# Kernel tuning notes

Measured on AMD Instinct MI355X. Metric: run time of the kernel, lower is better.

Reference implementation:

```python
import jax, jax.numpy as jnp
import numpy as np
import math

B, T, N_CTX, H = 4, 512, 2048, 1024
NUM_HEADS, NUM_INSTRUMENTS, MAX_BARS = 16, 16, 8
HEAD_DIM = H // NUM_HEADS


def setup_inputs() -> dict:
    key = jax.random.key(0)
    ks = jax.random.split(key, 16)
    s = 1.0 / math.sqrt(H)
    return {
        "query": jax.random.normal(ks[0], (B, T, H), jnp.float32),
        "context": jax.random.normal(ks[1], (B, N_CTX, H), jnp.float32),
        "instrument_ids": jax.random.randint(ks[2], (B, N_CTX), 0, NUM_INSTRUMENTS),
        "current_instrument_id": 3,
        "bar_offsets": jax.random.randint(ks[3], (B, N_CTX), 0, MAX_BARS),
        "Wq": jax.random.normal(ks[4], (H, H), jnp.float32) * s,
        "bq": jnp.zeros((H,), jnp.float32),
        "Wk": jax.random.normal(ks[5], (H, H), jnp.float32) * s,
        "bk": jnp.zeros((H,), jnp.float32),
        "Wv": jax.random.normal(ks[6], (H, H), jnp.float32) * s,
        "bv": jnp.zeros((H,), jnp.float32),
        "Wo": jax.random.normal(ks[7], (H, H), jnp.float32) * s,
        "bo": jnp.zeros((H,), jnp.float32),
        "inst_emb": jax.random.normal(ks[8], (NUM_INSTRUMENTS, H), jnp.float32),
        "bar_emb": jax.random.normal(ks[9], (MAX_BARS, H), jnp.float32),
    }


def reference(query, context, instrument_ids, current_instrument_id, bar_offsets,
              Wq, bq, Wk, bk, Wv, bv, Wo, bo, inst_emb, bar_emb):
    # current_instrument_id: python int -> broadcast to (B,)
    cur = jnp.full((B,), current_instrument_id, dtype=jnp.int64 if instrument_ids.dtype == jnp.int64 else jnp.int32)
    # add embeddings to query and context
    q = query + inst_emb[cur][:, None, :]                              # (B,T,H)
    ctx = context + inst_emb[instrument_ids] + bar_emb[jnp.clip(bar_offsets, 0, MAX_BARS - 1)]  # (B,N,H)
    # projections (torch Linear: x @ W.T + b)
    Q = (q @ Wq.T + bq).reshape(B, T, NUM_HEADS, HEAD_DIM).transpose(0, 2, 1, 3)      # (B,h,T,d)
    K = (ctx @ Wk.T + bk).reshape(B, N_CTX, NUM_HEADS, HEAD_DIM).transpose(0, 2, 1, 3)  # (B,h,N,d)
    V = (ctx @ Wv.T + bv).reshape(B, N_CTX, NUM_HEADS, HEAD_DIM).transpose(0, 2, 1, 3)  # (B,h,N,d)
    scores = jnp.einsum('bhtd,bhnd->bhtn', Q, K) / math.sqrt(HEAD_DIM)  # (B,h,T,N)
    # attend only to keys whose instrument differs from the current one
    keep = (instrument_ids != cur[:, None])[:, None, None, :]           # (B,1,1,N)
    scores = jnp.where(keep, scores, jnp.float32(-1e9))
    probs = jax.nn.softmax(scores, axis=-1)
    out = jnp.einsum('bhtn,bhnd->bhtd', probs, V).transpose(0, 2, 1, 3).reshape(B, T, H)
    return out @ Wo.T + bo
```

## Files before the change

### kernel.cpp

```cpp
#include <hip/hip_runtime.h>

#define H 1024
#define B_ 4
#define T_ 512
#define NCTX 2048
#define NH 16
#define HD 64

typedef __attribute__((ext_vector_type(8))) short bf16x8;
typedef __attribute__((ext_vector_type(4))) float f32x4;
typedef __attribute__((ext_vector_type(4))) short s16x4;

__device__ __forceinline__ ushort f2b(float f) {
  union { float f; unsigned u; } v; v.f = f;
  unsigned u = v.u;
  unsigned r = (u + 0x7FFFu + ((u >> 16) & 1u)) >> 16;
  return (ushort)r;
}

__device__ __forceinline__ unsigned cvt_pk_bf16(float lo, float hi) {
  unsigned r;
  asm("v_cvt_pk_bf16_f32 %0, %1, %2" : "=v"(r) : "v"(lo), "v"(hi));
  return r;
}

__device__ __forceinline__ void gld16(const void* g, void* l) {
  __builtin_amdgcn_global_load_lds((const __attribute__((address_space(1))) unsigned int*)g,
                                   (__attribute__((address_space(3))) unsigned int*)l, 16, 0, 0);
}


__global__ void prep_all(const float* __restrict__ query, const float* __restrict__ ctx,
                         const int* __restrict__ ids, const int* __restrict__ curp,
                         const int* __restrict__ bars,
                         const float* __restrict__ iemb, const float* __restrict__ bemb,
                         const float* __restrict__ Wq, const float* __restrict__ Wk,
                         const float* __restrict__ Wv, const float* __restrict__ Wo,
                         ushort* __restrict__ qin, ushort* __restrict__ ctxb,
                         ushort* __restrict__ Wqb, ushort* __restrict__ Wkb,
                         ushort* __restrict__ Wvb, ushort* __restrict__ Wob,
                         float* __restrict__ maskf) {
  for (int blk = blockIdx.x; blk < 14368; blk += gridDim.x) {
    if (blk < 8192) {
      int i = blk * 256 + threadIdx.x;
      int row = i >> 8;
      int c4 = i & 255;
      int id = ids[row];
      int bar = bars[row];
      bar = bar < 0 ? 0 : (bar > 7 ? 7 : bar);
      float4 v = ((const float4*)ctx)[i];
      float4 e = ((const float4*)(iemb + (size_t)id * H))[c4];
      float4 g = ((const float4*)(bemb + (size_t)bar * H))[c4];
      s16x4 o;
      o[0] = (short)f2b(v.x + e.x + g.x); o[1] = (short)f2b(v.y + e.y + g.y);
      o[2] = (short)f2b(v.z + e.z + g.z); o[3] = (short)f2b(v.w + e.w + g.w);
      ((s16x4*)ctxb)[i] = o;
    } else if (blk < 10240) {
      int cur = curp[0];
      int i = (blk - 8192) * 256 + threadIdx.x;
      int c4 = i & 255;
      float4 v = ((const float4*)query)[i];
      float4 e = ((const float4*)(iemb + (size_t)cur * H))[c4];
      s16x4 o;
      o[0] = (short)f2b(v.x + e.x); o[1] = (short)f2b(v.y + e.y);
      o[2] = (short)f2b(v.z + e.z); o[3] = (short)f2b(v.w + e.w);
      ((s16x4*)qin)[i] = o;
    } else if (blk < 14336) {
      int b2 = blk - 10240;
      int which = b2 >> 10;
      int i = (b2 & 1023) * 256 + threadIdx.x;
      const float* s = which == 0 ? Wq : which == 1 ? Wk : which == 2 ? Wv : Wo;
      ushort* d = which == 0 ? Wqb : which == 1 ? Wkb : which == 2 ? Wvb : Wob;
      float4 v = ((const float4*)s)[i];
      s16x4 o;
      o[0] = (short)f2b(v.x); o[1] = (short)f2b(v.y);
      o[2] = (short)f2b(v.z); o[3] = (short)f2b(v.w);
      ((s16x4*)d)[i] = o;
    } else {
      int cur = curp[0];
      int i = (blk - 14336) * 256 + threadIdx.x;
      maskf[i] = (ids[i] != cur) ? 0.f : -1e30f;
    }
  }
}


__global__ __launch_bounds__(256) void proj_k(const ushort* __restrict__ Aq,
                                              const ushort* __restrict__ Actx,
                                              const ushort* __restrict__ WQ,
                                              const ushort* __restrict__ WK,
                                              const ushort* __restrict__ WV,
                                              const float* __restrict__ bQ,
                                              const float* __restrict__ bK,
                                              const float* __restrict__ bV,
                                              ushort* __restrict__ Qout,
                                              ushort* __restrict__ Kout,
                                              ushort* __restrict__ VTout) {
  const int id = blockIdx.x;
  const ushort* A;
  const ushort* W;
  const float* bias;
  int row0, col0, mode;
  ushort* Cout;
  if (id < 1024) {
    int xcd = id & 7, rest = id >> 3;
    int bx = rest & 15, by = (rest >> 4) * 8 + xcd;
    A = Actx; row0 = by * 128;
    if (bx < 8) { W = WK; bias = bK; col0 = bx * 128; mode = 0; Cout = Kout; }
    else        { W = WV; bias = bV; col0 = (bx - 8) * 128; mode = 1; Cout = VTout; }
  } else {
    int q = id - 1024;
    A = Aq; row0 = (q >> 3) * 128; col0 = (q & 7) * 128;
    W = WQ; bias = bQ; mode = 2; Cout = Qout;
  }

  __shared__ ushort As[2][128 * 32];
  __shared__ ushort Bs[2][128 * 32];
  const int tid = threadIdx.x;
  const int lane = tid & 63;
  const int wv = tid >> 6;
  const int wr = wv >> 1, wc = wv & 1;
  const int lo = lane & 15, hi = lane >> 4;

  f32x4 acc[4][4];
#pragma unroll
  for (int m = 0; m < 4; m++)
#pragma unroll
    for (int n = 0; n < 4; n++) acc[m][n] = (f32x4){0.f, 0.f, 0.f, 0.f};

#pragma unroll
  for (int c = 0; c < 2; c++) {
    int ia = wv * 128 + c * 64 + lane;
    int r = ia >> 2, s = ia & 3;
    gld16(A + (size_t)(row0 + r) * H + s * 8, (char*)As[0] + (wv * 128 + c * 64) * 16);
    gld16(W + (size_t)(col0 + r) * H + s * 8, (char*)Bs[0] + (wv * 128 + c * 64) * 16);
  }
  __syncthreads();

  int cur = 0;
  for (int kt = 0; kt < 32; kt++) {
    if (kt < 31) {
#pragma unroll
      for (int c = 0; c < 2; c++) {
        int ia = wv * 128 + c * 64 + lane;
        int r = ia >> 2, s = ia & 3;
        gld16(A + (size_t)(row0 + r) * H + (kt + 1) * 32 + s * 8,
              (char*)As[cur ^ 1] + (wv * 128 + c * 64) * 16);
        gld16(W + (size_t)(col0 + r) * H + (kt + 1) * 32 + s * 8,
              (char*)Bs[cur ^ 1] + (wv * 128 + c * 64) * 16);
      }
    }
    bf16x8 af[4], bfr[4];
#pragma unroll
    for (int m = 0; m < 4; m++) af[m] = *(const bf16x8*)(As[cur] + (wr * 64 + m * 16 + lo) * 32 + hi * 8);
#pragma unroll
    for (int n = 0; n < 4; n++) bfr[n] = *(const bf16x8*)(Bs[cur] + (wc * 64 + n * 16 + lo) * 32 + hi * 8);
#pragma unroll
    for (int m = 0; m < 4; m++)
#pragma unroll
      for (int n = 0; n < 4; n++)
        acc[m][n] = __builtin_amdgcn_mfma_f32_16x16x32_bf16(af[m], bfr[n], acc[m][n], 0, 0, 0);
    __syncthreads();
    cur ^= 1;
  }

#pragma unroll
  for (int m = 0; m < 4; m++) {
    int gr0 = row0 + wr * 64 + m * 16 + hi * 4;
#pragma unroll
    for (int n = 0; n < 4; n++) {
      int gc = col0 + wc * 64 + n * 16 + lo;
      float bv = bias[gc];
      if (mode == 0) {
#pragma unroll
        for (int r = 0; r < 4; r++)
          Cout[(size_t)(gr0 + r) * H + gc] = f2b(acc[m][n][r] + bv);
      } else if (mode == 1) {
        int bb = gr0 >> 11, n0 = gr0 & 2047;
        s16x4 o;
#pragma unroll
        for (int r = 0; r < 4; r++) o[r] = (short)f2b(acc[m][n][r] + bv);
        *(s16x4*)(Cout + (size_t)bb * (H * NCTX) + (size_t)gc * NCTX + n0) = o;
      } else {
#pragma unroll
        for (int r = 0; r < 4; r++)
          Cout[(size_t)(gr0 + r) * H + gc] = f2b((acc[m][n][r] + bv) * 0.125f);
      }
    }
  }
}


__global__ __launch_bounds__(256) void gemm_o(const ushort* __restrict__ A,
                                              const ushort* __restrict__ W,
                                              const float* __restrict__ bias,
                                              float* __restrict__ Cout) {
  __shared__ ushort As[2][128 * 32];
  __shared__ ushort Bs[2][128 * 32];
  const int tid = threadIdx.x;
  const int lane = tid & 63;
  const int wv = tid >> 6;
  const int wr = wv >> 1, wc = wv & 1;
  const int lo = lane & 15, hi = lane >> 4;
  const int row0 = blockIdx.y * 128, col0 = blockIdx.x * 128;

  f32x4 acc[4][4];
#pragma unroll
  for (int m = 0; m < 4; m++)
#pragma unroll
    for (int n = 0; n < 4; n++) acc[m][n] = (f32x4){0.f, 0.f, 0.f, 0.f};

#pragma unroll
  for (int c = 0; c < 2; c++) {
    int ia = wv * 128 + c * 64 + lane;
    int r = ia >> 2, s = ia & 3;
    gld16(A + (size_t)(row0 + r) * H + s * 8, (char*)As[0] + (wv * 128 + c * 64) * 16);
    gld16(W + (size_t)(col0 + r) * H + s * 8, (char*)Bs[0] + (wv * 128 + c * 64) * 16);
  }
  __syncthreads();

  int cur = 0;
  for (int kt = 0; kt < 32; kt++) {
    if (kt < 31) {
#pragma unroll
      for (int c = 0; c < 2; c++) {
        int ia = wv * 128 + c * 64 + lane;
        int r = ia >> 2, s = ia & 3;
        gld16(A + (size_t)(row0 + r) * H + (kt + 1) * 32 + s * 8,
              (char*)As[cur ^ 1] + (wv * 128 + c * 64) * 16);
        gld16(W + (size_t)(col0 + r) * H + (kt + 1) * 32 + s * 8,
              (char*)Bs[cur ^ 1] + (wv * 128 + c * 64) * 16);
      }
    }
    bf16x8 af[4], bfr[4];
#pragma unroll
    for (int m = 0; m < 4; m++) af[m] = *(const bf16x8*)(As[cur] + (wr * 64 + m * 16 + lo) * 32 + hi * 8);
#pragma unroll
    for (int n = 0; n < 4; n++) bfr[n] = *(const bf16x8*)(Bs[cur] + (wc * 64 + n * 16 + lo) * 32 + hi * 8);
#pragma unroll
    for (int m = 0; m < 4; m++)
#pragma unroll
      for (int n = 0; n < 4; n++)
        acc[m][n] = __builtin_amdgcn_mfma_f32_16x16x32_bf16(af[m], bfr[n], acc[m][n], 0, 0, 0);
    __syncthreads();
    cur ^= 1;
  }

#pragma unroll
  for (int m = 0; m < 4; m++) {
    int gr0 = row0 + wr * 64 + m * 16 + hi * 4;
#pragma unroll
    for (int n = 0; n < 4; n++) {
      int gc = col0 + wc * 64 + n * 16 + lo;
      float bv = bias[gc];
#pragma unroll
      for (int r = 0; r < 4; r++)
        Cout[(size_t)(gr0 + r) * H + gc] = acc[m][n][r] + bv;
    }
  }
}


#define NSPLIT 2
#define KVLEN (NCTX / NSPLIT)
#define NT_KV (KVLEN / 64)

__global__ __launch_bounds__(256) void attn_k(const ushort* __restrict__ Q,
                                              const ushort* __restrict__ K,
                                              const ushort* __restrict__ VT,
                                              const float* __restrict__ maskf,
                                              float* __restrict__ OPf,
                                              float* __restrict__ mlf) {
  __shared__ ushort Ks[2][64 * 64];
  __shared__ ushort Vs[2][64 * 64];
  __shared__ ushort Ps[4][16 * 64];
  const int blk = (blockIdx.x & 7) * 128 + (blockIdx.x >> 3);
  const int qt = blk & 7;
  const int h = (blk >> 3) & 15;
  const int b = (blk >> 7) & 3;
  const int p = blk >> 9;
  const int tid = threadIdx.x, lane = tid & 63, w = tid >> 6;
  const int lo = lane & 15, hi = lane >> 4;
  const int swz = (lo & 7) << 4;
  const int kvbase = p * KVLEN;

  const ushort* Qp = Q + ((size_t)(b * T_ + qt * 64 + w * 16 + lo)) * H + h * HD;
  bf16x8 qf0 = *(const bf16x8*)(Qp + hi * 8);
  bf16x8 qf1 = *(const bf16x8*)(Qp + 32 + hi * 8);

  f32x4 oacc[4];
#pragma unroll
  for (int d = 0; d < 4; d++) oacc[d] = (f32x4){0.f, 0.f, 0.f, 0.f};
  float mrow = -1e30f, lrow = 0.f;

  const float* maskb = maskf + b * NCTX;
  const ushort* Kbase = K + ((size_t)(b * NCTX)) * H + h * HD;
  const ushort* Vbase = VT + (size_t)b * (H * NCTX) + (size_t)(h * HD) * NCTX;

  bf16x8 kr[2], vr[2];
#pragma unroll
  for (int i = 0; i < 2; i++) {
    int seg = tid + i * 256;
    int r = seg >> 3, s = seg & 7;
    kr[i] = *(const bf16x8*)(Kbase + (size_t)(kvbase + r) * H + s * 8);
    vr[i] = *(const bf16x8*)(Vbase + (size_t)r * NCTX + kvbase + s * 8);
  }
#pragma unroll
  for (int i = 0; i < 2; i++) {
    int seg = tid + i * 256;
    int r = seg >> 3, s = seg & 7;
    int wb = (r * 128 + s * 16) ^ ((r & 7) << 4);
    *(bf16x8*)((char*)Ks[0] + wb) = kr[i];
    *(bf16x8*)((char*)Vs[0] + wb) = vr[i];
  }
  __syncthreads();

  int curbuf = 0;
  for (int t = 0; t < NT_KV; t++) {
    int kvt = kvbase + t * 64;
    if (t < NT_KV - 1) {
#pragma unroll
      for (int i = 0; i < 2; i++) {
        int seg = tid + i * 256;
        int r = seg >> 3, s = seg & 7;
        kr[i] = *(const bf16x8*)(Kbase + (size_t)(kvt + 64 + r) * H + s * 8);
        vr[i] = *(const bf16x8*)(Vbase + (size_t)r * NCTX + kvt + 64 + s * 8);
      }
    }

    f32x4 sc[4];
    __builtin_amdgcn_s_setprio(1);
#pragma unroll
    for (int nt = 0; nt < 4; nt++) {
      bf16x8 kf0 = *(const bf16x8*)((char*)Ks[curbuf] + ((((nt * 16 + lo) * 128) + hi * 16) ^ swz));
      bf16x8 kf1 = *(const bf16x8*)((char*)Ks[curbuf] + ((((nt * 16 + lo) * 128) + 64 + hi * 16) ^ swz));
      f32x4 z = (f32x4){0.f, 0.f, 0.f, 0.f};
      z = __builtin_amdgcn_mfma_f32_16x16x32_bf16(kf0, qf0, z, 0, 0, 0);
      sc[nt] = __builtin_amdgcn_mfma_f32_16x16x32_bf16(kf1, qf1, z, 0, 0, 0);
    }
    __builtin_amdgcn_s_setprio(0);

    float pv[4][4];
#pragma unroll
    for (int nt = 0; nt < 4; nt++) {
      float4 mv = *(const float4*)(maskb + kvt + nt * 16 + hi * 4);
      pv[nt][0] = sc[nt][0] + mv.x;
      pv[nt][1] = sc[nt][1] + mv.y;
      pv[nt][2] = sc[nt][2] + mv.z;
      pv[nt][3] = sc[nt][3] + mv.w;
    }

    float m0 = fmaxf(fmaxf(pv[0][0], pv[0][1]), fmaxf(pv[0][2], pv[0][3]));
    float m1 = fmaxf(fmaxf(pv[1][0], pv[1][1]), fmaxf(pv[1][2], pv[1][3]));
    float m2 = fmaxf(fmaxf(pv[2][0], pv[2][1]), fmaxf(pv[2][2], pv[2][3]));
    float m3 = fmaxf(fmaxf(pv[3][0], pv[3][1]), fmaxf(pv[3][2], pv[3][3]));
    float x = fmaxf(fmaxf(m0, m1), fmaxf(m2, m3));
    x = fmaxf(x, __shfl_xor(x, 16));
    x = fmaxf(x, __shfl_xor(x, 32));
    bool defer = __all((x <= mrow + 8.0f) && (mrow > -1e29f));
    float mn, scal = 1.f;
    if (defer) {
      mn = mrow;
    } else {
      mn = fmaxf(mrow, x);
      scal = __expf(mrow - mn);
      mrow = mn;
    }
    float rsp[4];
#pragma unroll
    for (int nt = 0; nt < 4; nt++) {
      float e0 = __expf(pv[nt][0] - mn);
      float e1 = __expf(pv[nt][1] - mn);
      float e2 = __expf(pv[nt][2] - mn);
      float e3 = __expf(pv[nt][3] - mn);
      pv[nt][0] = e0; pv[nt][1] = e1; pv[nt][2] = e2; pv[nt][3] = e3;
      rsp[nt] = (e0 + e1) + (e2 + e3);
    }
    float rs = (rsp[0] + rsp[1]) + (rsp[2] + rsp[3]);
    rs += __shfl_xor(rs, 16);
    rs += __shfl_xor(rs, 32);
    if (defer) {
      lrow += rs;
    } else {
      lrow = lrow * scal + rs;
      float sq0 = __shfl(scal, hi * 4 + 0);
      float sq1 = __shfl(scal, hi * 4 + 1);
      float sq2 = __shfl(scal, hi * 4 + 2);
      float sq3 = __shfl(scal, hi * 4 + 3);
#pragma unroll
      for (int d = 0; d < 4; d++) {
        oacc[d][0] *= sq0; oacc[d][1] *= sq1; oacc[d][2] *= sq2; oacc[d][3] *= sq3;
      }
    }

#pragma unroll
    for (int nt = 0; nt < 4; nt++) {
      uint2 pw;
      pw.x = cvt_pk_bf16(pv[nt][0], pv[nt][1]);
      pw.y = cvt_pk_bf16(pv[nt][2], pv[nt][3]);
      *(uint2*)((char*)Ps[w] + ((lo * 128 + (nt * 16 + hi * 4) * 2) ^ swz)) = pw;
    }

    __builtin_amdgcn_s_setprio(1);
#pragma unroll
    for (int ks = 0; ks < 2; ks++) {
      bf16x8 pa = *(const bf16x8*)((char*)Ps[w] + ((lo * 128 + (ks * 64 + hi * 16)) ^ swz));
#pragma unroll
      for (int d = 0; d < 4; d++) {
        bf16x8 vf = *(const bf16x8*)((char*)Vs[curbuf] + (((d * 16 + lo) * 128 + ks * 64 + hi * 16) ^ swz));
        oacc[d] = __builtin_amdgcn_mfma_f32_16x16x32_bf16(pa, vf, oacc[d], 0, 0, 0);
      }
    }
    __builtin_amdgcn_s_setprio(0);

    if (t < NT_KV - 1) {
#pragma unroll
      for (int i = 0; i < 2; i++) {
        int seg = tid + i * 256;
        int r = seg >> 3, s = seg & 7;
        int wb = (r * 128 + s * 16) ^ ((r & 7) << 4);
        *(bf16x8*)((char*)Ks[curbuf ^ 1] + wb) = kr[i];
        *(bf16x8*)((char*)Vs[curbuf ^ 1] + wb) = vr[i];
      }
    }
    __syncthreads();
    curbuf ^= 1;
  }

  int row0 = b * 512 + qt * 64 + w * 16 + hi * 4;
#pragma unroll
  for (int d = 0; d < 4; d++) {
#pragma unroll
    for (int r = 0; r < 4; r++)
      OPf[((size_t)p * 2048 + row0 + r) * 1024 + h * 64 + d * 16 + lo] = oacc[d][r];
  }
  if (hi == 0) {
    int qrow = b * 512 + qt * 64 + w * 16 + lo;
    mlf[(((size_t)p * 2048 + qrow) * 16 + h) * 2] = mrow;
    mlf[(((size_t)p * 2048 + qrow) * 16 + h) * 2 + 1] = lrow;
  }
}

__global__ void attn_combine(const float* __restrict__ OPf, const float* __restrict__ mlf,
                             ushort* __restrict__ O) {
  int idx = blockIdx.x * 256 + threadIdx.x;
  int btr = idx >> 8;
  int c4 = idx & 255;
  int h = c4 >> 4;
  float m0 = mlf[((size_t)btr * 16 + h) * 2];
  float l0 = mlf[((size_t)btr * 16 + h) * 2 + 1];
  float m1 = mlf[(((size_t)2048 + btr) * 16 + h) * 2];
  float l1 = mlf[(((size_t)2048 + btr) * 16 + h) * 2 + 1];
  float M = fmaxf(m0, m1);
  float a0 = __expf(m0 - M), a1 = __expf(m1 - M);
  float inv = 1.0f / (a0 * l0 + a1 * l1);
  float4 o0 = ((const float4*)OPf)[idx];
  float4 o1 = ((const float4*)OPf)[(size_t)524288 + idx];
  s16x4 r;
  r[0] = (short)f2b((a0 * o0.x + a1 * o1.x) * inv);
  r[1] = (short)f2b((a0 * o0.y + a1 * o1.y) * inv);
  r[2] = (short)f2b((a0 * o0.z + a1 * o1.z) * inv);
  r[3] = (short)f2b((a0 * o0.w + a1 * o1.w) * inv);
  ((s16x4*)O)[idx] = r;
}


extern "C" void kernel_launch(void* const* d_in, const int* in_sizes, int n_in,
                              void* d_out, int out_size, void* d_ws, size_t ws_size,
                              hipStream_t stream) {
  const float* query = (const float*)d_in[0];
  const float* context = (const float*)d_in[1];
  const int* ids = (const int*)d_in[2];
  const int* curp = (const int*)d_in[3];
  const int* bars = (const int*)d_in[4];
  const float* Wq = (const float*)d_in[5];
  const float* bq = (const float*)d_in[6];
  const float* Wk = (const float*)d_in[7];
  const float* bk = (const float*)d_in[8];
  const float* Wv = (const float*)d_in[9];
  const float* bv = (const float*)d_in[10];
  const float* Wo = (const float*)d_in[11];
  const float* bo = (const float*)d_in[12];
  const float* iemb = (const float*)d_in[13];
  const float* bemb = (const float*)d_in[14];
  float* out = (float*)d_out;

  ushort* ws = (ushort*)d_ws;
  ushort* Wqb = ws;
  ushort* Wkb = Wqb + (1u << 20);
  ushort* Wvb = Wkb + (1u << 20);
  ushort* Wob = Wvb + (1u << 20);
  ushort* qin = Wob + (1u << 20);
  ushort* ctxb = qin + (2u << 20);
  ushort* Qb = ctxb + (8u << 20);
  ushort* Kb = Qb + (2u << 20);
  ushort* VTb = Kb + (8u << 20);
  ushort* AOb = VTb + (8u << 20);

  float* OPf = (float*)ctxb;
  float* mlf = (float*)qin;
  float* maskf = out;

  prep_all<<<2048, 256, 0, stream>>>(query, context, ids, curp, bars, iemb, bemb,
                                     Wq, Wk, Wv, Wo, qin, ctxb, Wqb, Wkb, Wvb, Wob, maskf);

  proj_k<<<1152, 256, 0, stream>>>(qin, ctxb, Wqb, Wkb, Wvb, bq, bk, bv, Qb, Kb, VTb);

  attn_k<<<1024, 256, 0, stream>>>(Qb, Kb, VTb, maskf, OPf, mlf);
  attn_combine<<<2048, 256, 0, stream>>>(OPf, mlf, AOb);

  gemm_o<<<dim3(8, 16), 256, 0, stream>>>(AOb, Wob, bo, out);
}
```

Before: 159.0 us.

## Load GEMM operands directly from global memory, dropping LDS staging

```diff
diff --git a/kernel.cpp b/kernel.cpp
--- a/kernel.cpp
+++ b/kernel.cpp
@@ -22,11 +22,6 @@
   unsigned r;
   asm("v_cvt_pk_bf16_f32 %0, %1, %2" : "=v"(r) : "v"(lo), "v"(hi));
   return r;
-}
-
-__device__ __forceinline__ void gld16(const void* g, void* l) {
-  __builtin_amdgcn_global_load_lds((const __attribute__((address_space(1))) unsigned int*)g,
-                                   (__attribute__((address_space(3))) unsigned int*)l, 16, 0, 0);
 }
 
 
@@ -114,8 +109,6 @@
     W = WQ; bias = bQ; mode = 2; Cout = Qout;
   }
 
-  __shared__ ushort As[2][128 * 32];
-  __shared__ ushort Bs[2][128 * 32];
   const int tid = threadIdx.x;
   const int lane = tid & 63;
   const int wv = tid >> 6;
@@ -128,40 +121,28 @@
 #pragma unroll
     for (int n = 0; n < 4; n++) acc[m][n] = (f32x4){0.f, 0.f, 0.f, 0.f};
 
-#pragma unroll
-  for (int c = 0; c < 2; c++) {
-    int ia = wv * 128 + c * 64 + lane;
-    int r = ia >> 2, s = ia & 3;
-    gld16(A + (size_t)(row0 + r) * H + s * 8, (char*)As[0] + (wv * 128 + c * 64) * 16);
-    gld16(W + (size_t)(col0 + r) * H + s * 8, (char*)Bs[0] + (wv * 128 + c * 64) * 16);
-  }
-  __syncthreads();
-
-  int cur = 0;
+  const ushort* Ap[4];
+  const ushort* Wp[4];
+#pragma unroll
+  for (int m = 0; m < 4; m++)
+    Ap[m] = A + (size_t)(row0 + wr * 64 + m * 16 + lo) * H + hi * 8;
+#pragma unroll
+  for (int n = 0; n < 4; n++)
+    Wp[n] = W + (size_t)(col0 + wc * 64 + n * 16 + lo) * H + hi * 8;
+
+#pragma unroll 4
   for (int kt = 0; kt < 32; kt++) {
-    if (kt < 31) {
-#pragma unroll
-      for (int c = 0; c < 2; c++) {
-        int ia = wv * 128 + c * 64 + lane;
-        int r = ia >> 2, s = ia & 3;
-        gld16(A + (size_t)(row0 + r) * H + (kt + 1) * 32 + s * 8,
-              (char*)As[cur ^ 1] + (wv * 128 + c * 64) * 16);
-        gld16(W + (size_t)(col0 + r) * H + (kt + 1) * 32 + s * 8,
-              (char*)Bs[cur ^ 1] + (wv * 128 + c * 64) * 16);
-      }
-    }
+    int ko = kt * 32;
     bf16x8 af[4], bfr[4];
 #pragma unroll
-    for (int m = 0; m < 4; m++) af[m] = *(const bf16x8*)(As[cur] + (wr * 64 + m * 16 + lo) * 32 + hi * 8);
-#pragma unroll
-    for (int n = 0; n < 4; n++) bfr[n] = *(const bf16x8*)(Bs[cur] + (wc * 64 + n * 16 + lo) * 32 + hi * 8);
+    for (int m = 0; m < 4; m++) af[m] = *(const bf16x8*)(Ap[m] + ko);
+#pragma unroll
+    for (int n = 0; n < 4; n++) bfr[n] = *(const bf16x8*)(Wp[n] + ko);
 #pragma unroll
     for (int m = 0; m < 4; m++)
 #pragma unroll
       for (int n = 0; n < 4; n++)
         acc[m][n] = __builtin_amdgcn_mfma_f32_16x16x32_bf16(af[m], bfr[n], acc[m][n], 0, 0, 0);
-    __syncthreads();
-    cur ^= 1;
   }
 
 #pragma unroll
@@ -195,8 +176,6 @@
                                               const ushort* __restrict__ W,
                                               const float* __restrict__ bias,
                                               float* __restrict__ Cout) {
-  __shared__ ushort As[2][128 * 32];
-  __shared__ ushort Bs[2][128 * 32];
   const int tid = threadIdx.x;
   const int lane = tid & 63;
   const int wv = tid >> 6;
@@ -210,40 +189,28 @@
 #pragma unroll
     for (int n = 0; n < 4; n++) acc[m][n] = (f32x4){0.f, 0.f, 0.f, 0.f};
 
-#pragma unroll
-  for (int c = 0; c < 2; c++) {
-    int ia = wv * 128 + c * 64 + lane;
-    int r = ia >> 2, s = ia & 3;
-    gld16(A + (size_t)(row0 + r) * H + s * 8, (char*)As[0] + (wv * 128 + c * 64) * 16);
-    gld16(W + (size_t)(col0 + r) * H + s * 8, (char*)Bs[0] + (wv * 128 + c * 64) * 16);
-  }
-  __syncthreads();
-
-  int cur = 0;
+  const ushort* Ap[4];
+  const ushort* Wp[4];
+#pragma unroll
+  for (int m = 0; m < 4; m++)
+    Ap[m] = A + (size_t)(row0 + wr * 64 + m * 16 + lo) * H + hi * 8;
+#pragma unroll
+  for (int n = 0; n < 4; n++)
+    Wp[n] = W + (size_t)(col0 + wc * 64 + n * 16 + lo) * H + hi * 8;
+
+#pragma unroll 4
   for (int kt = 0; kt < 32; kt++) {
-    if (kt < 31) {
-#pragma unroll
-      for (int c = 0; c < 2; c++) {
-        int ia = wv * 128 + c * 64 + lane;
-        int r = ia >> 2, s = ia & 3;
-        gld16(A + (size_t)(row0 + r) * H + (kt + 1) * 32 + s * 8,
-              (char*)As[cur ^ 1] + (wv * 128 + c * 64) * 16);
-        gld16(W + (size_t)(col0 + r) * H + (kt + 1) * 32 + s * 8,
-              (char*)Bs[cur ^ 1] + (wv * 128 + c * 64) * 16);
-      }
-    }
+    int ko = kt * 32;
     bf16x8 af[4], bfr[4];
 #pragma unroll
-    for (int m = 0; m < 4; m++) af[m] = *(const bf16x8*)(As[cur] + (wr * 64 + m * 16 + lo) * 32 + hi * 8);
-#pragma unroll
-    for (int n = 0; n < 4; n++) bfr[n] = *(const bf16x8*)(Bs[cur] + (wc * 64 + n * 16 + lo) * 32 + hi * 8);
+    for (int m = 0; m < 4; m++) af[m] = *(const bf16x8*)(Ap[m] + ko);
+#pragma unroll
+    for (int n = 0; n < 4; n++) bfr[n] = *(const bf16x8*)(Wp[n] + ko);
 #pragma unroll
     for (int m = 0; m < 4; m++)
 #pragma unroll
       for (int n = 0; n < 4; n++)
         acc[m][n] = __builtin_amdgcn_mfma_f32_16x16x32_bf16(af[m], bfr[n], acc[m][n], 0, 0, 0);
-    __syncthreads();
-    cur ^= 1;
   }
 
 #pragma unroll
```

After: 291.8 us. 1.84x slower.

## Process 128-key tiles per iteration in attention, dropping LDS double-buffering

Applied to the files above, without the earlier changes.

```diff
diff --git a/kernel.cpp b/kernel.cpp
--- a/kernel.cpp
+++ b/kernel.cpp
@@ -263,7 +263,7 @@
 
 #define NSPLIT 2
 #define KVLEN (NCTX / NSPLIT)
-#define NT_KV (KVLEN / 64)
+#define NT_KV (KVLEN / 128)
 
 __global__ __launch_bounds__(256) void attn_k(const ushort* __restrict__ Q,
                                               const ushort* __restrict__ K,
@@ -273,7 +273,7 @@
                                               float* __restrict__ mlf) {
   __shared__ ushort Ks[2][64 * 64];
   __shared__ ushort Vs[2][64 * 64];
-  __shared__ ushort Ps[4][16 * 64];
+  __shared__ ushort Ps[4][2][16 * 64];
   const int blk = (blockIdx.x & 7) * 128 + (blockIdx.x >> 3);
   const int qt = blk & 7;
   const int h = (blk >> 3) & 15;
@@ -297,64 +297,78 @@
   const ushort* Kbase = K + ((size_t)(b * NCTX)) * H + h * HD;
   const ushort* Vbase = VT + (size_t)b * (H * NCTX) + (size_t)(h * HD) * NCTX;
 
-  bf16x8 kr[2], vr[2];
-#pragma unroll
-  for (int i = 0; i < 2; i++) {
-    int seg = tid + i * 256;
-    int r = seg >> 3, s = seg & 7;
-    kr[i] = *(const bf16x8*)(Kbase + (size_t)(kvbase + r) * H + s * 8);
-    vr[i] = *(const bf16x8*)(Vbase + (size_t)r * NCTX + kvbase + s * 8);
-  }
-#pragma unroll
-  for (int i = 0; i < 2; i++) {
-    int seg = tid + i * 256;
-    int r = seg >> 3, s = seg & 7;
-    int wb = (r * 128 + s * 16) ^ ((r & 7) << 4);
-    *(bf16x8*)((char*)Ks[0] + wb) = kr[i];
-    *(bf16x8*)((char*)Vs[0] + wb) = vr[i];
+  const int sr = tid >> 3, ss = tid & 7;
+  const int wb0 = (sr * 128 + ss * 16) ^ ((sr & 7) << 4);
+  const int sr1 = (tid + 256) >> 3, ss1 = (tid + 256) & 7;
+  const int wb1 = (sr1 * 128 + ss1 * 16) ^ ((sr1 & 7) << 4);
+
+  bf16x8 kr[2][2], vr[2][2];
+#pragma unroll
+  for (int j = 0; j < 2; j++) {
+    int kv0 = kvbase + j * 64;
+    kr[j][0] = *(const bf16x8*)(Kbase + (size_t)(kv0 + sr) * H + ss * 8);
+    kr[j][1] = *(const bf16x8*)(Kbase + (size_t)(kv0 + sr1) * H + ss1 * 8);
+    vr[j][0] = *(const bf16x8*)(Vbase + (size_t)sr * NCTX + kv0 + ss * 8);
+    vr[j][1] = *(const bf16x8*)(Vbase + (size_t)sr1 * NCTX + kv0 + ss1 * 8);
+  }
+#pragma unroll
+  for (int j = 0; j < 2; j++) {
+    *(bf16x8*)((char*)Ks[j] + wb0) = kr[j][0];
+    *(bf16x8*)((char*)Ks[j] + wb1) = kr[j][1];
+    *(bf16x8*)((char*)Vs[j] + wb0) = vr[j][0];
+    *(bf16x8*)((char*)Vs[j] + wb1) = vr[j][1];
   }
   __syncthreads();
 
-  int curbuf = 0;
   for (int t = 0; t < NT_KV; t++) {
-    int kvt = kvbase + t * 64;
+    int kvt = kvbase + t * 128;
     if (t < NT_KV - 1) {
 #pragma unroll
-      for (int i = 0; i < 2; i++) {
-        int seg = tid + i * 256;
-        int r = seg >> 3, s = seg & 7;
-        kr[i] = *(const bf16x8*)(Kbase + (size_t)(kvt + 64 + r) * H + s * 8);
-        vr[i] = *(const bf16x8*)(Vbase + (size_t)r * NCTX + kvt + 64 + s * 8);
-      }
-    }
-
-    f32x4 sc[4];
+      for (int j = 0; j < 2; j++) {
+        int kv0 = kvt + 128 + j * 64;
+        kr[j][0] = *(const bf16x8*)(Kbase + (size_t)(kv0 + sr) * H + ss * 8);
+        kr[j][1] = *(const bf16x8*)(Kbase + (size_t)(kv0 + sr1) * H + ss1 * 8);
+        vr[j][0] = *(const bf16x8*)(Vbase + (size_t)sr * NCTX + kv0 + ss * 8);
+        vr[j][1] = *(const bf16x8*)(Vbase + (size_t)sr1 * NCTX + kv0 + ss1 * 8);
+      }
+    }
+
+    f32x4 sc[2][4];
     __builtin_amdgcn_s_setprio(1);
 #pragma unroll
-    for (int nt = 0; nt < 4; nt++) {
-      bf16x8 kf0 = *(const bf16x8*)((char*)Ks[curbuf] + ((((nt * 16 + lo) * 128) + hi * 16) ^ swz));
-      bf16x8 kf1 = *(const bf16x8*)((char*)Ks[curbuf] + ((((nt * 16 + lo) * 128) + 64 + hi * 16) ^ swz));
-      f32x4 z = (f32x4){0.f, 0.f, 0.f, 0.f};
-      z = __builtin_amdgcn_mfma_f32_16x16x32_bf16(kf0, qf0, z, 0, 0, 0);
-      sc[nt] = __builtin_amdgcn_mfma_f32_16x16x32_bf16(kf1, qf1, z, 0, 0, 0);
-    }
+    for (int j = 0; j < 2; j++)
+#pragma unroll
+      for (int nt = 0; nt < 4; nt++) {
+        bf16x8 kf0 = *(const bf16x8*)((char*)Ks[j] + ((((nt * 16 + lo) * 128) + hi * 16) ^ swz));
+        bf16x8 kf1 = *(const bf16x8*)((char*)Ks[j] + ((((nt * 16 + lo) * 128) + 64 + hi * 16) ^ swz));
+        f32x4 z = (f32x4){0.f, 0.f, 0.f, 0.f};
+        z = __builtin_amdgcn_mfma_f32_16x16x32_bf16(kf0, qf0, z, 0, 0, 0);
+        sc[j][nt] = __builtin_amdgcn_mfma_f32_16x16x32_bf16(kf1, qf1, z, 0, 0, 0);
+      }
     __builtin_amdgcn_s_setprio(0);
 
-    float pv[4][4];
-#pragma unroll
-    for (int nt = 0; nt < 4; nt++) {
-      float4 mv = *(const float4*)(maskb + kvt + nt * 16 + hi * 4);
-      pv[nt][0] = sc[nt][0] + mv.x;
-      pv[nt][1] = sc[nt][1] + mv.y;
-      pv[nt][2] = sc[nt][2] + mv.z;
-      pv[nt][3] = sc[nt][3] + mv.w;
-    }
-
-    float m0 = fmaxf(fmaxf(pv[0][0], pv[0][1]), fmaxf(pv[0][2], pv[0][3]));
-    float m1 = fmaxf(fmaxf(pv[1][0], pv[1][1]), fmaxf(pv[1][2], pv[1][3]));
-    float m2 = fmaxf(fmaxf(pv[2][0], pv[2][1]), fmaxf(pv[2][2], pv[2][3]));
-    float m3 = fmaxf(fmaxf(pv[3][0], pv[3][1]), fmaxf(pv[3][2], pv[3][3]));
-    float x = fmaxf(fmaxf(m0, m1), fmaxf(m2, m3));
+    float pv[2][4][4];
+#pragma unroll
+    for (int j = 0; j < 2; j++)
+#pragma unroll
+      for (int nt = 0; nt < 4; nt++) {
+        float4 mv = *(const float4*)(maskb + kvt + j * 64 + nt * 16 + hi * 4);
+        pv[j][nt][0] = sc[j][nt][0] + mv.x;
+        pv[j][nt][1] = sc[j][nt][1] + mv.y;
+        pv[j][nt][2] = sc[j][nt][2] + mv.z;
+        pv[j][nt][3] = sc[j][nt][3] + mv.w;
+      }
+
+    float gm[2];
+#pragma unroll
+    for (int j = 0; j < 2; j++) {
+      float m0 = fmaxf(fmaxf(pv[j][0][0], pv[j][0][1]), fmaxf(pv[j][0][2], pv[j][0][3]));
+      float m1 = fmaxf(fmaxf(pv[j][1][0], pv[j][1][1]), fmaxf(pv[j][1][2], pv[j][1][3]));
+      float m2 = fmaxf(fmaxf(pv[j][2][0], pv[j][2][1]), fmaxf(pv[j][2][2], pv[j][2][3]));
+      float m3 = fmaxf(fmaxf(pv[j][3][0], pv[j][3][1]), fmaxf(pv[j][3][2], pv[j][3][3]));
+      gm[j] = fmaxf(fmaxf(m0, m1), fmaxf(m2, m3));
+    }
+    float x = fmaxf(gm[0], gm[1]);
     x = fmaxf(x, __shfl_xor(x, 16));
     x = fmaxf(x, __shfl_xor(x, 32));
     bool defer = __all((x <= mrow + 8.0f) && (mrow > -1e29f));
@@ -366,17 +380,21 @@
       scal = __expf(mrow - mn);
       mrow = mn;
     }
-    float rsp[4];
-#pragma unroll
-    for (int nt = 0; nt < 4; nt++) {
-      float e0 = __expf(pv[nt][0] - mn);
-      float e1 = __expf(pv[nt][1] - mn);
-      float e2 = __expf(pv[nt][2] - mn);
-      float e3 = __expf(pv[nt][3] - mn);
-      pv[nt][0] = e0; pv[nt][1] = e1; pv[nt][2] = e2; pv[nt][3] = e3;
-      rsp[nt] = (e0 + e1) + (e2 + e3);
-    }
-    float rs = (rsp[0] + rsp[1]) + (rsp[2] + rsp[3]);
+    float rs = 0.f;
+#pragma unroll
+    for (int j = 0; j < 2; j++) {
+      float rsp[4];
+#pragma unroll
+      for (int nt = 0; nt < 4; nt++) {
+        float e0 = __expf(pv[j][nt][0] - mn);
+        float e1 = __expf(pv[j][nt][1] - mn);
+        float e2 = __expf(pv[j][nt][2] - mn);
+        float e3 = __expf(pv[j][nt][3] - mn);
+        pv[j][nt][0] = e0; pv[j][nt][1] = e1; pv[j][nt][2] = e2; pv[j][nt][3] = e3;
+        rsp[nt] = (e0 + e1) + (e2 + e3);
+      }
+      rs += (rsp[0] + rsp[1]) + (rsp[2] + rsp[3]);
+    }
     rs += __shfl_xor(rs, 16);
     rs += __shfl_xor(rs, 32);
     if (defer) {
@@ -394,37 +412,40 @@
     }
 
 #pragma unroll
-    for (int nt = 0; nt < 4; nt++) {
-      uint2 pw;
-      pw.x = cvt_pk_bf16(pv[nt][0], pv[nt][1]);
-      pw.y = cvt_pk_bf16(pv[nt][2], pv[nt][3]);
-      *(uint2*)((char*)Ps[w] + ((lo * 128 + (nt * 16 + hi * 4) * 2) ^ swz)) = pw;
-    }
+    for (int j = 0; j < 2; j++)
+#pragma unroll
+      for (int nt = 0; nt < 4; nt++) {
+        uint2 pw;
+        pw.x = cvt_pk_bf16(pv[j][nt][0], pv[j][nt][1]);
+        pw.y = cvt_pk_bf16(pv[j][nt][2], pv[j][nt][3]);
+        *(uint2*)((char*)Ps[w][j] + ((lo * 128 + (nt * 16 + hi * 4) * 2) ^ swz)) = pw;
+      }
 
     __builtin_amdgcn_s_setprio(1);
 #pragma unroll
-    for (int ks = 0; ks < 2; ks++) {
-      bf16x8 pa = *(const bf16x8*)((char*)Ps[w] + ((lo * 128 + (ks * 64 + hi * 16)) ^ swz));
-#pragma unroll
-      for (int d = 0; d < 4; d++) {
-        bf16x8 vf = *(const bf16x8*)((char*)Vs[curbuf] + (((d * 16 + lo) * 128 + ks * 64 + hi * 16) ^ swz));
-        oacc[d] = __builtin_amdgcn_mfma_f32_16x16x32_bf16(pa, vf, oacc[d], 0, 0, 0);
-      }
-    }
+    for (int j = 0; j < 2; j++)
+#pragma unroll
+      for (int ks = 0; ks < 2; ks++) {
+        bf16x8 pa = *(const bf16x8*)((char*)Ps[w][j] + ((lo * 128 + (ks * 64 + hi * 16)) ^ swz));
+#pragma unroll
+        for (int d = 0; d < 4; d++) {
+          bf16x8 vf = *(const bf16x8*)((char*)Vs[j] + (((d * 16 + lo) * 128 + ks * 64 + hi * 16) ^ swz));
+          oacc[d] = __builtin_amdgcn_mfma_f32_16x16x32_bf16(pa, vf, oacc[d], 0, 0, 0);
+        }
+      }
     __builtin_amdgcn_s_setprio(0);
 
     if (t < NT_KV - 1) {
-#pragma unroll
-      for (int i = 0; i < 2; i++) {
-        int seg = tid + i * 256;
-        int r = seg >> 3, s = seg & 7;
-        int wb = (r * 128 + s * 16) ^ ((r & 7) << 4);
-        *(bf16x8*)((char*)Ks[curbuf ^ 1] + wb) = kr[i];
-        *(bf16x8*)((char*)Vs[curbuf ^ 1] + wb) = vr[i];
-      }
-    }
-    __syncthreads();
-    curbuf ^= 1;
+      __syncthreads();
+#pragma unroll
+      for (int j = 0; j < 2; j++) {
+        *(bf16x8*)((char*)Ks[j] + wb0) = kr[j][0];
+        *(bf16x8*)((char*)Ks[j] + wb1) = kr[j][1];
+        *(bf16x8*)((char*)Vs[j] + wb0) = vr[j][0];
+        *(bf16x8*)((char*)Vs[j] + wb1) = vr[j][1];
+      }
+      __syncthreads();
+    }
   }
 
   int row0 = b * 512 + qt * 64 + w * 16 + hi * 4;
```

Measured after the change: 153.3 us. 1.04x faster.
